# Kernel optimization log

Hardware: AMD Instinct MI355X
Metric: run time of the kernel (lower is better)

Reference implementation:

```python
import jax, jax.numpy as jnp
import numpy as np

N, E = 50000, 800000
NFEAT, HID, NHEAD, NCLASS = 256, 32, 8, 40
NEG_SLOPE = 0.2


def gat_conv(x, src, dst, W, a_src, a_dst, bias, heads, out_ch, concat):
    n = x.shape[0]
    h = (x @ W).reshape(n, heads, out_ch)              # [N, H, C]
    alpha_src = jnp.einsum('nhc,hc->nh', h, a_src)     # [N, H]
    alpha_dst = jnp.einsum('nhc,hc->nh', h, a_dst)
    e = jax.nn.leaky_relu(alpha_src[src] + alpha_dst[dst], NEG_SLOPE)  # [E, H]
    # segment softmax over incoming edges of each dst node
    m = jax.ops.segment_max(e, dst, num_segments=n)
    ex = jnp.exp(e - m[dst])
    s = jax.ops.segment_sum(ex, dst, num_segments=n)
    alpha = ex / (s[dst] + 1e-16)                      # [E, H]
    out = jax.ops.segment_sum(h[src] * alpha[:, :, None], dst, num_segments=n)  # [N, H, C]
    out = out.reshape(n, heads * out_ch) if concat else out.mean(axis=1)
    return out + bias


def setup_inputs() -> dict:
    key = jax.random.key(0)
    ks = jax.random.split(key, 12)
    x = jax.random.normal(ks[0], (N, NFEAT), dtype=jnp.float32)
    edge_index = jax.random.randint(ks[1], (2, E), 0, N, dtype=jnp.int64)
    edge_attr = jax.random.normal(ks[2], (E, 8), dtype=jnp.float32)  # unused by the model
    s1 = 1.0 / np.sqrt(NFEAT)
    s2 = 1.0 / np.sqrt(HID * NHEAD)
    W1 = jax.random.normal(ks[3], (NFEAT, NHEAD * HID), dtype=jnp.float32) * s1
    att_src1 = jax.random.normal(ks[4], (NHEAD, HID), dtype=jnp.float32) * 0.1
    att_dst1 = jax.random.normal(ks[5], (NHEAD, HID), dtype=jnp.float32) * 0.1
    b1 = jnp.zeros((NHEAD * HID,), dtype=jnp.float32)
    W2 = jax.random.normal(ks[6], (NHEAD * HID, NCLASS), dtype=jnp.float32) * s2
    att_src2 = jax.random.normal(ks[7], (1, NCLASS), dtype=jnp.float32) * 0.1
    att_dst2 = jax.random.normal(ks[8], (1, NCLASS), dtype=jnp.float32) * 0.1
    b2 = jnp.zeros((NCLASS,), dtype=jnp.float32)
    return {"x": x, "edge_index": edge_index, "edge_attr": edge_attr,
            "W1": W1, "att_src1": att_src1, "att_dst1": att_dst1, "b1": b1,
            "W2": W2, "att_src2": att_src2, "att_dst2": att_dst2, "b2": b2}


def reference(x, edge_index, edge_attr, W1, att_src1, att_dst1, b1, W2, att_src2, att_dst2, b2):
    # eval mode: dropout is identity. GATConv adds self-loops by default.
    n = x.shape[0]
    loops = jnp.arange(n, dtype=edge_index.dtype)
    src = jnp.concatenate([edge_index[0], loops])
    dst = jnp.concatenate([edge_index[1], loops])
    h = jax.nn.elu(gat_conv(x, src, dst, W1, att_src1, att_dst1, b1, NHEAD, HID, True))
    final = gat_conv(h, src, dst, W2, att_src2, att_dst2, b2, 1, NCLASS, False)
    return final, jax.nn.log_softmax(final, axis=1)
```

## Files before the change

### kernel.cpp

```cpp
#include <hip/hip_runtime.h>
#include <hip/hip_bf16.h>
#include <hip/hip_fp16.h>
#include <math.h>

#define NN 50000
#define EE 800000
#define ET 850000
#define F1 256
#define NHEAD 8
#define HID 32
#define NCLASS 40
#define NEG 0.2f

typedef __attribute__((ext_vector_type(8))) _Float16 half8_t;
typedef __attribute__((ext_vector_type(4))) float float4_t;

__device__ __forceinline__ int clampN(int v) {
    return v < 0 ? 0 : (v >= NN ? NN - 1 : v);
}
__device__ __forceinline__ unsigned short f2h(float f) {
    __half h = __float2half(f);
    return __builtin_bit_cast(unsigned short, h);
}
__device__ __forceinline__ float h2f(unsigned short u) {
    __half h = __builtin_bit_cast(__half, u);
    return __half2float(h);
}
__device__ __forceinline__ float hlo2f(unsigned int u) {
    return h2f((unsigned short)(u & 0xFFFFu));
}
__device__ __forceinline__ float hhi2f(unsigned int u) {
    return h2f((unsigned short)(u >> 16));
}

__global__ __launch_bounds__(256) void hist_kernel(const int* __restrict__ ei, int* __restrict__ deg,
                                                   unsigned int* __restrict__ pack) {
    int t = blockIdx.x * 256 + threadIdx.x;
    if (t >= ET) return;
    int d = (t < EE) ? ei[EE + t] : (t - EE);
    d = clampN(d);
    int r = atomicAdd(&deg[d], 1);
    pack[t] = ((unsigned)d << 15) | (unsigned)r;
}

__global__ __launch_bounds__(256) void scan1_kernel(const int* __restrict__ deg, int* __restrict__ off, int* __restrict__ bsum) {
    __shared__ int lds[256];
    int b = blockIdx.x, tid = threadIdx.x;
    int base = b * 1024 + tid * 4;
    int v0 = (base + 0 < NN) ? deg[base + 0] : 0;
    int v1 = (base + 1 < NN) ? deg[base + 1] : 0;
    int v2 = (base + 2 < NN) ? deg[base + 2] : 0;
    int v3 = (base + 3 < NN) ? deg[base + 3] : 0;
    int s1 = v0 + v1, s2 = s1 + v2, s3 = s2 + v3;
    lds[tid] = s3;
    __syncthreads();
    for (int o = 1; o < 256; o <<= 1) {
        int t = (tid >= o) ? lds[tid - o] : 0;
        __syncthreads();
        if (tid >= o) lds[tid] += t;
        __syncthreads();
    }
    int excl = tid ? lds[tid - 1] : 0;
    if (base + 0 < NN) off[base + 1] = excl + v0;
    if (base + 1 < NN) off[base + 2] = excl + s1;
    if (base + 2 < NN) off[base + 3] = excl + s2;
    if (base + 3 < NN) off[base + 4] = excl + s3;
    if (tid == 255) bsum[b] = lds[255];
}

__global__ __launch_bounds__(256) void scan2_kernel(int* __restrict__ bsum, int nb) {
    __shared__ int lds[256];
    int tid = threadIdx.x;
    lds[tid] = (tid < nb) ? bsum[tid] : 0;
    __syncthreads();
    for (int o = 1; o < 256; o <<= 1) {
        int t = (tid >= o) ? lds[tid - o] : 0;
        __syncthreads();
        if (tid >= o) lds[tid] += t;
        __syncthreads();
    }
    if (tid < nb) bsum[tid] = lds[tid];
}

__global__ __launch_bounds__(256) void scan3_kernel(int* __restrict__ off, const int* __restrict__ bsum) {
    int b = blockIdx.x, tid = threadIdx.x;
    if (b == 0 && tid == 0) off[0] = 0;
    if (b == 0) return;
    int add = bsum[b - 1];
    int base = b * 1024 + tid * 4;
    #pragma unroll
    for (int i = 0; i < 4; ++i) {
        if (base + i < NN) off[base + i + 1] += add;
    }
}

__global__ __launch_bounds__(256) void scatter_kernel(const int* __restrict__ ei, const int* __restrict__ off,
                                                      const unsigned int* __restrict__ pack, int* __restrict__ esrc) {
    int t = blockIdx.x * 256 + threadIdx.x;
    if (t >= ET) return;
    unsigned p = pack[t];
    int d = p >> 15;
    int r = p & 0x7FFF;
    int s = (t < EE) ? ei[t] : (t - EE);
    s = clampN(s);
    esrc[off[d] + r] = s;
}

__global__ __launch_bounds__(256) void prep_kernel(const float* __restrict__ W1,
                                                   const float* __restrict__ as1, const float* __restrict__ ad1,
                                                   unsigned short* __restrict__ Bt) {
    int n = blockIdx.x;
    int k = threadIdx.x;
    float v;
    if (n < 256) {
        v = W1[(size_t)k * 256 + n];
    } else {
        int j = n - 256;
        int h = j & 7;
        const float* att = (j < 8) ? (as1 + h * 32) : (ad1 + h * 32);
        float s = 0.f;
        #pragma unroll
        for (int c = 0; c < 32; ++c) s += W1[(size_t)k * 256 + h * 32 + c] * att[c];
        v = s;
    }
    Bt[n * 256 + k] = f2h(v);
}

#define AKP 40
__global__ __launch_bounds__(256, 2) void gemm1_kernel(const float* __restrict__ x,
                                                       const unsigned short* __restrict__ Bt,
                                                       unsigned short* __restrict__ h1b,
                                                       float* __restrict__ asrc1, float* __restrict__ adst1) {
    __shared__ __align__(16) unsigned short Ah[128 * AKP];
    __shared__ __align__(16) unsigned short Bs[272 * AKP];
    int tid = threadIdx.x;
    int wave = tid >> 6, lane = tid & 63;
    int quad = lane >> 4, l16 = lane & 15;
    int row0 = blockIdx.x * 128;

    float4_t acc[2][17];
    #pragma unroll
    for (int i = 0; i < 2; ++i)
        #pragma unroll
        for (int j = 0; j < 17; ++j) acc[i][j] = (float4_t){0.f, 0.f, 0.f, 0.f};

    for (int k0 = 0; k0 < 256; k0 += 32) {
        __syncthreads();
        #pragma unroll
        for (int i = 0; i < 4; ++i) {
            int id = i * 256 + tid;
            int r = id >> 3, kq = id & 7;
            int rr = row0 + r; if (rr >= NN) rr = NN - 1;
            float4 v = *(const float4*)(x + (size_t)rr * 256 + k0 + kq * 4);
            ushort4 hi;
            hi.x = f2h(v.x);
            hi.y = f2h(v.y);
            hi.z = f2h(v.z);
            hi.w = f2h(v.w);
            *(ushort4*)(Ah + r * AKP + kq * 4) = hi;
        }
        for (int id = tid; id < 272 * 4; id += 256) {
            int r = id >> 2, kq = id & 3;
            *(float4*)(Bs + r * AKP + kq * 8) = *(const float4*)(Bt + (size_t)r * 256 + k0 + kq * 8);
        }
        __syncthreads();
        half8_t ah[2];
        #pragma unroll
        for (int mt = 0; mt < 2; ++mt) {
            int mrow = wave * 32 + mt * 16 + l16;
            ah[mt] = *(const half8_t*)(Ah + mrow * AKP + quad * 8);
        }
        #pragma unroll
        for (int nt = 0; nt < 17; ++nt) {
            int nrow = nt * 16 + l16;
            half8_t bh = *(const half8_t*)(Bs + nrow * AKP + quad * 8);
            #pragma unroll
            for (int mt = 0; mt < 2; ++mt) {
                acc[mt][nt] = __builtin_amdgcn_mfma_f32_16x16x32_f16(ah[mt], bh, acc[mt][nt], 0, 0, 0);
            }
        }
    }
    #pragma unroll
    for (int mt = 0; mt < 2; ++mt) {
        int rbase = row0 + wave * 32 + mt * 16 + quad * 4;
        #pragma unroll
        for (int r = 0; r < 4; ++r) {
            int row = rbase + r;
            if (row >= NN) continue;
            #pragma unroll
            for (int nt = 0; nt < 16; ++nt)
                h1b[(size_t)row * 256 + nt * 16 + l16] = f2h(acc[mt][nt][r]);
            float v = acc[mt][16][r];
            if (l16 < 8) asrc1[row * 8 + l16] = v;
            else         adst1[row * 8 + (l16 - 8)] = v;
        }
    }
}

#define WST 68
__global__ __launch_bounds__(256) void agg1_kernel(const unsigned short* __restrict__ h1b, const float* __restrict__ asrc,
                                                   const float* __restrict__ adst, const int* __restrict__ esrc,
                                                   const int* __restrict__ off,
                                                   const float* __restrict__ b1, unsigned short* __restrict__ hout) {
    __shared__ __align__(16) float wl[4][8 * WST];
    __shared__ __align__(16) int  snl[4][64];
    int tid = threadIdx.x;
    int wave = tid >> 6;
    int wid = blockIdx.x * 4 + wave;
    if (wid >= NN) return;
    int lane = tid & 63;
    int hp = lane & 7;
    int jp = lane >> 3;
    int hc = lane >> 3;
    int c0 = lane * 4;
    float* wlw = wl[wave];
    int* snw = snl[wave];
    const float* wrow = wlw + hc * WST;
    const char* hb = (const char*)h1b;
    unsigned lofs = (unsigned)c0 * 2;
    float adh_p = adst[wid * 8 + hp];
    int e0 = off[wid], e1 = off[wid + 1];

    float m = -INFINITY, s = 0.f;
    float ax = 0.f, ay = 0.f, az = 0.f, aw = 0.f;

    for (int base = e0; base < e1; base += 64) {
        int cnt = e1 - base; if (cnt > 64) cnt = 64;
        int snv = esrc[base + (lane < cnt ? lane : cnt - 1)];
        snw[lane] = snv;
        int nch = (cnt + 7) >> 3;
        float ee[8];
        float wmax = -INFINITY;
        #pragma unroll
        for (int cj = 0; cj < 8; ++cj) {
            if (cj >= nch) { ee[cj] = -INFINITY; continue; }
            int jedge = cj * 8 + jp;
            int sj = __shfl(snv, jedge);
            float a = asrc[sj * 8 + hp];
            float e = a + adh_p;
            e = (e >= 0.f) ? e : NEG * e;
            if (jedge >= cnt) e = -INFINITY;
            ee[cj] = e;
            wmax = fmaxf(wmax, e);
        }
        wmax = fmaxf(wmax, __shfl_xor(wmax, 8));
        wmax = fmaxf(wmax, __shfl_xor(wmax, 16));
        wmax = fmaxf(wmax, __shfl_xor(wmax, 32));
        float mn = fmaxf(m, wmax);
        float t = __expf(m - mn);
        m = mn;
        s *= t;
        float tc = __shfl(t, hc);
        ax *= tc; ay *= tc; az *= tc; aw *= tc;
        #pragma unroll
        for (int cj = 0; cj < 8; ++cj) {
            if (cj >= nch) break;
            float w = __expf(ee[cj] - mn);
            s += w;
            wlw[hp * WST + cj * 8 + jp] = w;
        }
        int nslots = nch * 8;
        for (int j = 0; j < nslots; j += 8) {
            float4 wa = *(const float4*)(wrow + j);
            float4 wb = *(const float4*)(wrow + j + 4);
            int4 sa = *(const int4*)(snw + j);
            int4 sb = *(const int4*)(snw + j + 4);
            const char* r0 = hb + ((size_t)(unsigned)__builtin_amdgcn_readfirstlane(sa.x) << 9);
            const char* r1 = hb + ((size_t)(unsigned)__builtin_amdgcn_readfirstlane(sa.y) << 9);
            const char* r2 = hb + ((size_t)(unsigned)__builtin_amdgcn_readfirstlane(sa.z) << 9);
            const char* r3 = hb + ((size_t)(unsigned)__builtin_amdgcn_readfirstlane(sa.w) << 9);
            const char* r4 = hb + ((size_t)(unsigned)__builtin_amdgcn_readfirstlane(sb.x) << 9);
            const char* r5 = hb + ((size_t)(unsigned)__builtin_amdgcn_readfirstlane(sb.y) << 9);
            const char* r6 = hb + ((size_t)(unsigned)__builtin_amdgcn_readfirstlane(sb.z) << 9);
            const char* r7 = hb + ((size_t)(unsigned)__builtin_amdgcn_readfirstlane(sb.w) << 9);
            uint2 u0 = *(const uint2*)(r0 + lofs);
            uint2 u1 = *(const uint2*)(r1 + lofs);
            uint2 u2 = *(const uint2*)(r2 + lofs);
            uint2 u3 = *(const uint2*)(r3 + lofs);
            uint2 u4 = *(const uint2*)(r4 + lofs);
            uint2 u5 = *(const uint2*)(r5 + lofs);
            uint2 u6 = *(const uint2*)(r6 + lofs);
            uint2 u7 = *(const uint2*)(r7 + lofs);
            ax += wa.x * hlo2f(u0.x);
            ay += wa.x * hhi2f(u0.x);
            az += wa.x * hlo2f(u0.y);
            aw += wa.x * hhi2f(u0.y);
            ax += wa.y * hlo2f(u1.x);
            ay += wa.y * hhi2f(u1.x);
            az += wa.y * hlo2f(u1.y);
            aw += wa.y * hhi2f(u1.y);
            ax += wa.z * hlo2f(u2.x);
            ay += wa.z * hhi2f(u2.x);
            az += wa.z * hlo2f(u2.y);
            aw += wa.z * hhi2f(u2.y);
            ax += wa.w * hlo2f(u3.x);
            ay += wa.w * hhi2f(u3.x);
            az += wa.w * hlo2f(u3.y);
            aw += wa.w * hhi2f(u3.y);
            ax += wb.x * hlo2f(u4.x);
            ay += wb.x * hhi2f(u4.x);
            az += wb.x * hlo2f(u4.y);
            aw += wb.x * hhi2f(u4.y);
            ax += wb.y * hlo2f(u5.x);
            ay += wb.y * hhi2f(u5.x);
            az += wb.y * hlo2f(u5.y);
            aw += wb.y * hhi2f(u5.y);
            ax += wb.z * hlo2f(u6.x);
            ay += wb.z * hhi2f(u6.x);
            az += wb.z * hlo2f(u6.y);
            aw += wb.z * hhi2f(u6.y);
            ax += wb.w * hlo2f(u7.x);
            ay += wb.w * hhi2f(u7.x);
            az += wb.w * hlo2f(u7.y);
            aw += wb.w * hhi2f(u7.y);
        }
    }
    s += __shfl_xor(s, 8);
    s += __shfl_xor(s, 16);
    s += __shfl_xor(s, 32);
    float sh = __shfl(s, hc);
    float inv = 1.f / (sh + 1e-16f);
    float4 b = *(const float4*)(b1 + c0);
    float vx = ax * inv + b.x, vy = ay * inv + b.y, vz = az * inv + b.z, vw = aw * inv + b.w;
    ushort4 o;
    o.x = f2h((vx > 0.f) ? vx : expm1f(vx));
    o.y = f2h((vy > 0.f) ? vy : expm1f(vy));
    o.z = f2h((vz > 0.f) ? vz : expm1f(vz));
    o.w = f2h((vw > 0.f) ? vw : expm1f(vw));
    *(ushort4*)(hout + (size_t)wid * 256 + c0) = o;
}

#define G2_TM 128
#define G2_KC 32
__global__ __launch_bounds__(256) void gemm2_kernel(const unsigned short* __restrict__ h, const float* __restrict__ W2,
                                                    const float* __restrict__ at_s, const float* __restrict__ at_d,
                                                    unsigned short* __restrict__ h2b, float* __restrict__ as2,
                                                    float* __restrict__ ad2) {
    __shared__ __align__(16) float w2s[256 * 40];
    __shared__ __align__(16) float As[G2_KC][132];
    int tid = threadIdx.x;
    for (int i = tid; i < 256 * 40; i += 256) w2s[i] = W2[i];
    int g  = tid & 7;
    int rg = tid >> 3;
    int row0 = blockIdx.x * G2_TM;
    float acc[4][5] = {};
    float ats[5], atd[5];
    #pragma unroll
    for (int j = 0; j < 5; ++j) { ats[j] = at_s[g + 8 * j]; atd[j] = at_d[g + 8 * j]; }

    for (int k0 = 0; k0 < 256; k0 += G2_KC) {
        __syncthreads();
        #pragma unroll
        for (int i = 0; i < 2; ++i) {
            int id = i * 256 + tid;
            int r  = id >> 2;
            int kq = id & 3;
            int rr = row0 + r; if (rr >= NN) rr = NN - 1;
            uint4 u = *(const uint4*)(h + (size_t)rr * 256 + k0 + kq * 8);
            As[kq * 8 + 0][r] = hlo2f(u.x);
            As[kq * 8 + 1][r] = hhi2f(u.x);
            As[kq * 8 + 2][r] = hlo2f(u.y);
            As[kq * 8 + 3][r] = hhi2f(u.y);
            As[kq * 8 + 4][r] = hlo2f(u.z);
            As[kq * 8 + 5][r] = hhi2f(u.z);
            As[kq * 8 + 6][r] = hlo2f(u.w);
            As[kq * 8 + 7][r] = hhi2f(u.w);
        }
        __syncthreads();
        #pragma unroll 4
        for (int k = 0; k < G2_KC; ++k) {
            float4 a = *(const float4*)(&As[k][rg * 4]);
            float w[5];
            #pragma unroll
            for (int j = 0; j < 5; ++j) w[j] = w2s[(k0 + k) * 40 + g + 8 * j];
            float av[4] = {a.x, a.y, a.z, a.w};
            #pragma unroll
            for (int r = 0; r < 4; ++r)
                #pragma unroll
                for (int j = 0; j < 5; ++j)
                    acc[r][j] += av[r] * w[j];
        }
    }

    #pragma unroll
    for (int r = 0; r < 4; ++r) {
        int row = row0 + rg * 4 + r;
        float ps = 0.f, pd = 0.f;
        #pragma unroll
        for (int j = 0; j < 5; ++j) {
            ps += acc[r][j] * ats[j];
            pd += acc[r][j] * atd[j];
        }
        ps += __shfl_xor(ps, 1); pd += __shfl_xor(pd, 1);
        ps += __shfl_xor(ps, 2); pd += __shfl_xor(pd, 2);
        ps += __shfl_xor(ps, 4); pd += __shfl_xor(pd, 4);
        if (row < NN) {
            #pragma unroll
            for (int j = 0; j < 5; ++j) h2b[(size_t)row * 40 + g + 8 * j] = f2h(acc[r][j]);
            if (g == 0) { as2[row] = ps; ad2[row] = pd; }
        }
    }
}

__global__ __launch_bounds__(256) void agg2_kernel(const unsigned short* __restrict__ h2b, const float* __restrict__ asrc,
                                                   const float* __restrict__ adst, const int* __restrict__ esrc,
                                                   const int* __restrict__ off,
                                                   const float* __restrict__ b2, float* __restrict__ outF,
                                                   float* __restrict__ outL) {
    __shared__ __align__(16) float wl2[4][64];
    __shared__ __align__(16) int  snl2[4][64];
    int tid = threadIdx.x;
    int wave = tid >> 6;
    int wid = blockIdx.x * 4 + wave;
    if (wid >= NN) return;
    int lane = tid & 63;
    int c = lane;
    const char* hb = (const char*)h2b;
    unsigned coff = (unsigned)(c < NCLASS ? c : 0) * 2;
    float* wlw = wl2[wave];
    int* snw = snl2[wave];
    float bc = (c < NCLASS) ? b2[c] : 0.f;
    float adh = adst[wid];
    int e0 = off[wid], e1 = off[wid + 1];

    float m = -INFINITY, s = 0.f, acc = 0.f;

    for (int base = e0; base < e1; base += 64) {
        int cnt = e1 - base; if (cnt > 64) cnt = 64;
        int snv = esrc[base + (lane < cnt ? lane : cnt - 1)];
        snw[lane] = snv;
        float a = asrc[snv];
        float e = a + adh;
        e = (e >= 0.f) ? e : NEG * e;
        if (lane >= cnt) e = -INFINITY;
        float cm = e;
        cm = fmaxf(cm, __shfl_xor(cm, 1));
        cm = fmaxf(cm, __shfl_xor(cm, 2));
        cm = fmaxf(cm, __shfl_xor(cm, 4));
        cm = fmaxf(cm, __shfl_xor(cm, 8));
        cm = fmaxf(cm, __shfl_xor(cm, 16));
        cm = fmaxf(cm, __shfl_xor(cm, 32));
        float mn = fmaxf(m, cm);
        float t = __expf(m - mn);
        float w = __expf(e - mn);
        s = s * t + w;
        m = mn;
        wlw[lane] = w;
        acc *= t;
        int n8 = (cnt + 7) & ~7;
        for (int j = 0; j < n8; j += 8) {
            float4 wa = *(const float4*)(wlw + j);
            float4 wb = *(const float4*)(wlw + j + 4);
            int4 sa = *(const int4*)(snw + j);
            int4 sb = *(const int4*)(snw + j + 4);
            const char* r0 = hb + (size_t)((unsigned)__builtin_amdgcn_readfirstlane(sa.x) * 80u);
            const char* r1 = hb + (size_t)((unsigned)__builtin_amdgcn_readfirstlane(sa.y) * 80u);
            const char* r2 = hb + (size_t)((unsigned)__builtin_amdgcn_readfirstlane(sa.z) * 80u);
            const char* r3 = hb + (size_t)((unsigned)__builtin_amdgcn_readfirstlane(sa.w) * 80u);
            const char* r4 = hb + (size_t)((unsigned)__builtin_amdgcn_readfirstlane(sb.x) * 80u);
            const char* r5 = hb + (size_t)((unsigned)__builtin_amdgcn_readfirstlane(sb.y) * 80u);
            const char* r6 = hb + (size_t)((unsigned)__builtin_amdgcn_readfirstlane(sb.z) * 80u);
            const char* r7 = hb + (size_t)((unsigned)__builtin_amdgcn_readfirstlane(sb.w) * 80u);
            unsigned short v0 = *(const unsigned short*)(r0 + coff);
            unsigned short v1 = *(const unsigned short*)(r1 + coff);
            unsigned short v2 = *(const unsigned short*)(r2 + coff);
            unsigned short v3 = *(const unsigned short*)(r3 + coff);
            unsigned short v4 = *(const unsigned short*)(r4 + coff);
            unsigned short v5 = *(const unsigned short*)(r5 + coff);
            unsigned short v6 = *(const unsigned short*)(r6 + coff);
            unsigned short v7 = *(const unsigned short*)(r7 + coff);
            acc += wa.x * h2f(v0);
            acc += wa.y * h2f(v1);
            acc += wa.z * h2f(v2);
            acc += wa.w * h2f(v3);
            acc += wb.x * h2f(v4);
            acc += wb.y * h2f(v5);
            acc += wb.z * h2f(v6);
            acc += wb.w * h2f(v7);
        }
    }
    s += __shfl_xor(s, 1);
    s += __shfl_xor(s, 2);
    s += __shfl_xor(s, 4);
    s += __shfl_xor(s, 8);
    s += __shfl_xor(s, 16);
    s += __shfl_xor(s, 32);
    float inv = 1.f / (s + 1e-16f);
    float fin = (c < NCLASS) ? (acc * inv + bc) : -INFINITY;
    if (c < NCLASS) outF[(size_t)wid * 40 + c] = fin;
    float mx = fin;
    for (int o = 32; o; o >>= 1) mx = fmaxf(mx, __shfl_xor(mx, o));
    float ex = (c < NCLASS) ? __expf(fin - mx) : 0.f;
    float sm = ex;
    for (int o = 32; o; o >>= 1) sm += __shfl_xor(sm, o);
    if (c < NCLASS) outL[(size_t)wid * 40 + c] = fin - mx - __logf(sm);
}

extern "C" void kernel_launch(void* const* d_in, const int* in_sizes, int n_in,
                              void* d_out, int out_size, void* d_ws, size_t ws_size,
                              hipStream_t stream) {
    const float* x   = (const float*)d_in[0];
    const int*   ei  = (const int*)d_in[1];
    const float* W1  = (const float*)d_in[3];
    const float* as1 = (const float*)d_in[4];
    const float* ad1 = (const float*)d_in[5];
    const float* b1  = (const float*)d_in[6];
    const float* W2  = (const float*)d_in[7];
    const float* as2c = (const float*)d_in[8];
    const float* ad2c = (const float*)d_in[9];
    const float* b2  = (const float*)d_in[10];

    float* outF = (float*)d_out;
    float* outL = outF + (size_t)NN * NCLASS;

    char* w = (char*)d_ws;
    auto alloc = [&](size_t bytes) {
        void* p = (void*)w;
        w += (bytes + 255) & ~(size_t)255;
        return p;
    };
    unsigned short* h1b = (unsigned short*)alloc((size_t)NN * 256 * 2);
    unsigned short* hbuf = (unsigned short*)alloc((size_t)NN * 256 * 2);
    unsigned short* h2b = (unsigned short*)alloc((size_t)NN * 40 * 2);
    float* asrc1 = (float*)alloc((size_t)NN * 8 * 4);
    float* adst1 = (float*)alloc((size_t)NN * 8 * 4);
    float* asrc2 = (float*)alloc((size_t)NN * 4);
    float* adst2 = (float*)alloc((size_t)NN * 4);
    int* deg    = (int*)alloc((size_t)NN * 4);
    int* off    = (int*)alloc((size_t)(NN + 1) * 4);
    unsigned int* pack = (unsigned int*)alloc((size_t)ET * 4);
    int* esrc   = (int*)alloc((size_t)ET * 4);
    int* bsum   = (int*)alloc(64 * 4);
    unsigned short* W1th = (unsigned short*)alloc((size_t)272 * 256 * 2);

    const int NB_SCAN = (NN + 1023) / 1024;

    hipMemsetAsync(deg, 0, (size_t)NN * 4, stream);

    hist_kernel<<<(ET + 255) / 256, 256, 0, stream>>>(ei, deg, pack);
    scan1_kernel<<<NB_SCAN, 256, 0, stream>>>(deg, off, bsum);
    scan2_kernel<<<1, 256, 0, stream>>>(bsum, NB_SCAN);
    scan3_kernel<<<NB_SCAN, 256, 0, stream>>>(off, bsum);
    scatter_kernel<<<(ET + 255) / 256, 256, 0, stream>>>(ei, off, pack, esrc);

    prep_kernel<<<272, 256, 0, stream>>>(W1, as1, ad1, W1th);
    gemm1_kernel<<<(NN + 127) / 128, 256, 0, stream>>>(x, W1th, h1b, asrc1, adst1);
    agg1_kernel<<<(NN + 3) / 4, 256, 0, stream>>>(h1b, asrc1, adst1, esrc, off, b1, hbuf);
    gemm2_kernel<<<(NN + G2_TM - 1) / G2_TM, 256, 0, stream>>>(hbuf, W2, as2c, ad2c, h2b, asrc2, adst2);
    agg2_kernel<<<(NN + 3) / 4, 256, 0, stream>>>(h2b, asrc2, adst2, esrc, off, b2, outF, outL);
}
```

Before: 341.7 us.

## Use MFMA fp16 for layer-2 GEMM with attention vectors folded into weights

```diff
diff --git a/kernel.cpp b/kernel.cpp
--- a/kernel.cpp
+++ b/kernel.cpp
@@ -124,6 +124,24 @@
         v = s;
     }
     Bt[n * 256 + k] = f2h(v);
+}
+
+__global__ __launch_bounds__(256) void prep2_kernel(const float* __restrict__ W2,
+                                                    const float* __restrict__ ats, const float* __restrict__ atd,
+                                                    unsigned short* __restrict__ Bt2) {
+    int n = blockIdx.x;
+    int k = threadIdx.x;
+    float v = 0.f;
+    if (n < NCLASS) {
+        v = W2[(size_t)k * NCLASS + n];
+    } else if (n == NCLASS) {
+        #pragma unroll
+        for (int j = 0; j < NCLASS; ++j) v += W2[(size_t)k * NCLASS + j] * ats[j];
+    } else if (n == NCLASS + 1) {
+        #pragma unroll
+        for (int j = 0; j < NCLASS; ++j) v += W2[(size_t)k * NCLASS + j] * atd[j];
+    }
+    Bt2[n * 256 + k] = f2h(v);
 }
 
 #define AKP 40
@@ -330,74 +348,69 @@
     *(ushort4*)(hout + (size_t)wid * 256 + c0) = o;
 }
 
-#define G2_TM 128
-#define G2_KC 32
-__global__ __launch_bounds__(256) void gemm2_kernel(const unsigned short* __restrict__ h, const float* __restrict__ W2,
-                                                    const float* __restrict__ at_s, const float* __restrict__ at_d,
-                                                    unsigned short* __restrict__ h2b, float* __restrict__ as2,
-                                                    float* __restrict__ ad2) {
-    __shared__ __align__(16) float w2s[256 * 40];
-    __shared__ __align__(16) float As[G2_KC][132];
+#define BKP 40
+__global__ __launch_bounds__(256, 2) void gemm2_kernel(const unsigned short* __restrict__ h,
+                                                       const unsigned short* __restrict__ Bt2,
+                                                       unsigned short* __restrict__ h2b, float* __restrict__ as2,
+                                                       float* __restrict__ ad2) {
+    __shared__ __align__(16) unsigned short Ah[128 * BKP];
+    __shared__ __align__(16) unsigned short Bs[48 * BKP];
     int tid = threadIdx.x;
-    for (int i = tid; i < 256 * 40; i += 256) w2s[i] = W2[i];
-    int g  = tid & 7;
-    int rg = tid >> 3;
-    int row0 = blockIdx.x * G2_TM;
-    float acc[4][5] = {};
-    float ats[5], atd[5];
+    int wave = tid >> 6, lane = tid & 63;
+    int quad = lane >> 4, l16 = lane & 15;
+    int row0 = blockIdx.x * 128;
+
+    float4_t acc[2][3];
     #pragma unroll
-    for (int j = 0; j < 5; ++j) { ats[j] = at_s[g + 8 * j]; atd[j] = at_d[g + 8 * j]; }
-
-    for (int k0 = 0; k0 < 256; k0 += G2_KC) {
+    for (int i = 0; i < 2; ++i)
+        #pragma unroll
+        for (int j = 0; j < 3; ++j) acc[i][j] = (float4_t){0.f, 0.f, 0.f, 0.f};
+
+    for (int k0 = 0; k0 < 256; k0 += 32) {
         __syncthreads();
         #pragma unroll
         for (int i = 0; i < 2; ++i) {
             int id = i * 256 + tid;
-            int r  = id >> 2;
-            int kq = id & 3;
+            int r = id >> 2, kq = id & 3;
             int rr = row0 + r; if (rr >= NN) rr = NN - 1;
-            uint4 u = *(const uint4*)(h + (size_t)rr * 256 + k0 + kq * 8);
-            As[kq * 8 + 0][r] = hlo2f(u.x);
-            As[kq * 8 + 1][r] = hhi2f(u.x);
-            As[kq * 8 + 2][r] = hlo2f(u.y);
-            As[kq * 8 + 3][r] = hhi2f(u.y);
-            As[kq * 8 + 4][r] = hlo2f(u.z);
-            As[kq * 8 + 5][r] = hhi2f(u.z);
-            As[kq * 8 + 6][r] = hlo2f(u.w);
-            As[kq * 8 + 7][r] = hhi2f(u.w);
-        }
-        __syncthreads();
-        #pragma unroll 4
-        for (int k = 0; k < G2_KC; ++k) {
-            float4 a = *(const float4*)(&As[k][rg * 4]);
-            float w[5];
+            *(float4*)(Ah + r * BKP + kq * 8) = *(const float4*)(h + (size_t)rr * 256 + k0 + kq * 8);
+        }
+        if (tid < 192) {
+            int r = tid >> 2, kq = tid & 3;
+            *(float4*)(Bs + r * BKP + kq * 8) = *(const float4*)(Bt2 + (size_t)r * 256 + k0 + kq * 8);
+        }
+        __syncthreads();
+        half8_t ah[2];
+        #pragma unroll
+        for (int mt = 0; mt < 2; ++mt) {
+            int mrow = wave * 32 + mt * 16 + l16;
+            ah[mt] = *(const half8_t*)(Ah + mrow * BKP + quad * 8);
+        }
+        #pragma unroll
+        for (int nt = 0; nt < 3; ++nt) {
+            int nrow = nt * 16 + l16;
+            half8_t bh = *(const half8_t*)(Bs + nrow * BKP + quad * 8);
             #pragma unroll
-            for (int j = 0; j < 5; ++j) w[j] = w2s[(k0 + k) * 40 + g + 8 * j];
-            float av[4] = {a.x, a.y, a.z, a.w};
+            for (int mt = 0; mt < 2; ++mt) {
+                acc[mt][nt] = __builtin_amdgcn_mfma_f32_16x16x32_f16(ah[mt], bh, acc[mt][nt], 0, 0, 0);
+            }
+        }
+    }
+    #pragma unroll
+    for (int mt = 0; mt < 2; ++mt) {
+        int rbase = row0 + wave * 32 + mt * 16 + quad * 4;
+        #pragma unroll
+        for (int r = 0; r < 4; ++r) {
+            int row = rbase + r;
+            if (row >= NN) continue;
             #pragma unroll
-            for (int r = 0; r < 4; ++r)
-                #pragma unroll
-                for (int j = 0; j < 5; ++j)
-                    acc[r][j] += av[r] * w[j];
-        }
-    }
-
-    #pragma unroll
-    for (int r = 0; r < 4; ++r) {
-        int row = row0 + rg * 4 + r;
-        float ps = 0.f, pd = 0.f;
-        #pragma unroll
-        for (int j = 0; j < 5; ++j) {
-            ps += acc[r][j] * ats[j];
-            pd += acc[r][j] * atd[j];
-        }
-        ps += __shfl_xor(ps, 1); pd += __shfl_xor(pd, 1);
-        ps += __shfl_xor(ps, 2); pd += __shfl_xor(pd, 2);
-        ps += __shfl_xor(ps, 4); pd += __shfl_xor(pd, 4);
-        if (row < NN) {
-            #pragma unroll
-            for (int j = 0; j < 5; ++j) h2b[(size_t)row * 40 + g + 8 * j] = f2h(acc[r][j]);
-            if (g == 0) { as2[row] = ps; ad2[row] = pd; }
+            for (int nt = 0; nt < 3; ++nt) {
+                int j = nt * 16 + l16;
+                float v = acc[mt][nt][r];
+                if (j < NCLASS)            h2b[(size_t)row * 40 + j] = f2h(v);
+                else if (j == NCLASS)      as2[row] = v;
+                else if (j == NCLASS + 1)  ad2[row] = v;
+            }
         }
     }
 }
@@ -532,6 +545,7 @@
     int* esrc   = (int*)alloc((size_t)ET * 4);
     int* bsum   = (int*)alloc(64 * 4);
     unsigned short* W1th = (unsigned short*)alloc((size_t)272 * 256 * 2);
+    unsigned short* W2t  = (unsigned short*)alloc((size_t)48 * 256 * 2);
 
     const int NB_SCAN = (NN + 1023) / 1024;
 
@@ -544,8 +558,9 @@
     scatter_kernel<<<(ET + 255) / 256, 256, 0, stream>>>(ei, off, pack, esrc);
 
     prep_kernel<<<272, 256, 0, stream>>>(W1, as1, ad1, W1th);
+    prep2_kernel<<<48, 256, 0, stream>>>(W2, as2c, ad2c, W2t);
     gemm1_kernel<<<(NN + 127) / 128, 256, 0, stream>>>(x, W1th, h1b, asrc1, adst1);
     agg1_kernel<<<(NN + 3) / 4, 256, 0, stream>>>(h1b, asrc1, adst1, esrc, off, b1, hbuf);
-    gemm2_kernel<<<(NN + G2_TM - 1) / G2_TM, 256, 0, stream>>>(hbuf, W2, as2c, ad2c, h2b, asrc2, adst2);
+    gemm2_kernel<<<(NN + 127) / 128, 256, 0, stream>>>(hbuf, W2t, h2b, asrc2, adst2);
     agg2_kernel<<<(NN + 3) / 4, 256, 0, stream>>>(h2b, asrc2, adst2, esrc, off, b2, outF, outL);
 }
```

Result: faster. 323.6 us (-5.3%).
